# Kernel optimization log

Hardware: AMD Instinct MI355X
Metric: run time of the kernel (lower is better)

The kernel has to match this reference:

```python
import jax, jax.numpy as jnp
import numpy as np

NV = 16384
NF = 32768
B = 4


def _build_laplacian(nv, nf, seed=0):
    # Faithful replication of the torch module's __init__ laplacian construction.
    rng = np.random.RandomState(seed)
    faces = rng.randint(0, nv, size=(nf, 3)).astype(np.int64)
    lap = np.zeros((nv, nv), dtype=np.float32)
    lap[faces[:, 0], faces[:, 1]] = -1
    lap[faces[:, 1], faces[:, 0]] = -1
    lap[faces[:, 1], faces[:, 2]] = -1
    lap[faces[:, 2], faces[:, 1]] = -1
    lap[faces[:, 2], faces[:, 0]] = -1
    lap[faces[:, 0], faces[:, 2]] = -1
    r, c = np.diag_indices(nv)
    lap[r, c] = -lap.sum(1)
    deg = lap[r, c]  # degree per vertex (>= 0)
    # vectorized version of: for i: if lap[i,i] > 0: lap[i,:] /= lap[i,i]
    scale = np.where(deg > 0, 1.0 / np.maximum(deg, 1.0), 1.0).astype(np.float32)
    lap = lap * scale[:, None]
    return lap


def setup_inputs() -> dict:
    key = jax.random.key(0)
    x = jax.random.normal(key, (B, NV, 3), dtype=jnp.float32)
    laplacian = jnp.asarray(_build_laplacian(NV, NF))
    return {"x": x, "laplacian": laplacian}


def reference(x, laplacian):
    # y[b, i, d] = sum_j L[i, j] * x[b, j, d]
    y = jnp.einsum("ij,bjd->bid", laplacian, x)
    # squared L2 norm per batch element (sum over all non-batch dims)
    loss = jnp.sum(y * y, axis=(1, 2))  # [B]
    return loss
```

## Files before the change

### kernel.cpp

```cpp
#include <hip/hip_runtime.h>

#define NV 16384
#define BROWS 32
#define JT 256
#define NT (NV / JT)
#define THREADS 256

typedef const __attribute__((address_space(1))) void* as1_ptr;
typedef __attribute__((address_space(3))) void* as3_ptr;

__device__ __forceinline__ void gload_lds16(const float* g, float* l) {
  __builtin_amdgcn_global_load_lds((as1_ptr)g, (as3_ptr)l, 16, 0, 0);
}

#define FENCE asm volatile("" ::: "memory")
#define WAITV(n) asm volatile("s_waitcnt vmcnt(" #n ")" ::: "memory")

__global__ __launch_bounds__(THREADS, 2) void lap_loss_kernel(
    const float* __restrict__ x, const float* __restrict__ L,
    float* __restrict__ out) {
  __shared__ float lbuf[2][BROWS][JT];

  const int lane = threadIdx.x & 63;
  const int w    = threadIdx.x >> 6;
  const size_t i0 = (size_t)blockIdx.x * BROWS;

  const float* gL[8];
#pragma unroll
  for (int r = 0; r < 8; ++r)
    gL[r] = L + (i0 + 8 * w + r) * NV + lane * 4;

  const float* gx = x + (size_t)w * NV * 3 + lane * 12;

  float acc[BROWS][3];
#pragma unroll
  for (int r = 0; r < BROWS; ++r)
#pragma unroll
    for (int d = 0; d < 3; ++d) acc[r][d] = 0.f;

  float4 xc0 = *(const float4*)(gx + 0);
  float4 xc1 = *(const float4*)(gx + 4);
  float4 xc2 = *(const float4*)(gx + 8);
  FENCE;
#pragma unroll
  for (int r = 0; r < 8; ++r)
    gload_lds16(gL[r], &lbuf[0][8 * w + r][0]);
  FENCE;

#pragma unroll 1
  for (int t = 0; t < NT; ++t) {
    const int cur = t & 1;

    float4 xn0, xn1, xn2;
    if (t + 1 < NT) {
#pragma unroll
      for (int r = 0; r < 8; ++r)
        gload_lds16(gL[r] + (size_t)(t + 1) * JT, &lbuf[cur ^ 1][8 * w + r][0]);
      FENCE;
      const float* gxn = gx + (size_t)(t + 1) * JT * 3;
      xn0 = *(const float4*)(gxn + 0);
      xn1 = *(const float4*)(gxn + 4);
      xn2 = *(const float4*)(gxn + 8);
      FENCE;
      WAITV(11);
    } else {
      WAITV(0);
    }
    __builtin_amdgcn_s_barrier();
    FENCE;

    {
      const float xf[12] = {xc0.x, xc0.y, xc0.z, xc0.w,
                            xc1.x, xc1.y, xc1.z, xc1.w,
                            xc2.x, xc2.y, xc2.z, xc2.w};
#pragma unroll
      for (int r = 0; r < BROWS; ++r) {
        float4 lv = *(const float4*)&lbuf[cur][r][lane * 4];
        const float lf[4] = {lv.x, lv.y, lv.z, lv.w};
#pragma unroll
        for (int jj = 0; jj < 4; ++jj)
#pragma unroll
          for (int d = 0; d < 3; ++d)
            acc[r][d] = fmaf(lf[jj], xf[jj * 3 + d], acc[r][d]);
      }
    }

    FENCE;
    __builtin_amdgcn_s_barrier();
    FENCE;

    xc0 = xn0; xc1 = xn1; xc2 = xn2;
  }

  float s = 0.f;
#pragma unroll
  for (int r = 0; r < BROWS; ++r)
#pragma unroll
    for (int d = 0; d < 3; ++d) {
      float v = acc[r][d];
#pragma unroll
      for (int off = 32; off > 0; off >>= 1)
        v += __shfl_xor(v, off, 64);
      s += v * v;
    }

  if (lane == 0) atomicAdd(&out[w], s);
}

extern "C" void kernel_launch(void* const* d_in, const int* in_sizes, int n_in,
                              void* d_out, int out_size, void* d_ws, size_t ws_size,
                              hipStream_t stream) {
  const float* x = (const float*)d_in[0];
  const float* L = (const float*)d_in[1];
  float* out = (float*)d_out;

  hipMemsetAsync(out, 0, out_size * sizeof(float), stream);

  const int nblocks = NV / BROWS;
  lap_loss_kernel<<<nblocks, THREADS, 0, stream>>>(x, L, out);
}
```

Baseline: 229.3 us.

## Deepen L-tile prefetch to four stages and halve rows per block

Replaces the double-buffered LDS pipeline with a four-slot ring buffer that keeps three tiles in flight, issuing each tile three iterations ahead and waiting with matching vmcnt counts. Rows per block drop from 32 to 16, which doubles the grid and halves the accumulator registers. The aim is to hide more HBM latency on this bandwidth-bound streaming of the dense Laplacian. In exchange, x is now re-read by twice as many blocks and the hand-counted waitcnt values must exactly match the number of outstanding loads.

```diff
diff --git a/kernel.cpp b/kernel.cpp
--- a/kernel.cpp
+++ b/kernel.cpp
@@ -1,7 +1,7 @@
 #include <hip/hip_runtime.h>
 
 #define NV 16384
-#define BROWS 32
+#define BROWS 16
 #define JT 256
 #define NT (NV / JT)
 #define THREADS 256
@@ -15,20 +15,21 @@
 
 #define FENCE asm volatile("" ::: "memory")
 #define WAITV(n) asm volatile("s_waitcnt vmcnt(" #n ")" ::: "memory")
+#define BARRIER __builtin_amdgcn_s_barrier()
 
 __global__ __launch_bounds__(THREADS, 2) void lap_loss_kernel(
     const float* __restrict__ x, const float* __restrict__ L,
     float* __restrict__ out) {
-  __shared__ float lbuf[2][BROWS][JT];
+  __shared__ float lbuf[4][BROWS][JT];
 
   const int lane = threadIdx.x & 63;
   const int w    = threadIdx.x >> 6;
   const size_t i0 = (size_t)blockIdx.x * BROWS;
 
-  const float* gL[8];
-#pragma unroll
-  for (int r = 0; r < 8; ++r)
-    gL[r] = L + (i0 + 8 * w + r) * NV + lane * 4;
+  const float* gL0 = L + (i0 + 4 * w + 0) * NV + lane * 4;
+  const float* gL1 = L + (i0 + 4 * w + 1) * NV + lane * 4;
+  const float* gL2 = L + (i0 + 4 * w + 2) * NV + lane * 4;
+  const float* gL3 = L + (i0 + 4 * w + 3) * NV + lane * 4;
 
   const float* gx = x + (size_t)w * NV * 3 + lane * 12;
 
@@ -38,59 +39,72 @@
 #pragma unroll
     for (int d = 0; d < 3; ++d) acc[r][d] = 0.f;
 
-  float4 xc0 = *(const float4*)(gx + 0);
-  float4 xc1 = *(const float4*)(gx + 4);
-  float4 xc2 = *(const float4*)(gx + 8);
-  FENCE;
-#pragma unroll
-  for (int r = 0; r < 8; ++r)
-    gload_lds16(gL[r], &lbuf[0][8 * w + r][0]);
-  FENCE;
+  float4 xpf[4][3];
+
+#define ISSUE(T, S) do {                                               \
+    const float4* _p = (const float4*)(gx + (size_t)(T) * JT * 3);     \
+    xpf[S][0] = _p[0]; xpf[S][1] = _p[1]; xpf[S][2] = _p[2];           \
+    FENCE;                                                             \
+    gload_lds16(gL0 + (size_t)(T) * JT, &lbuf[S][4 * w + 0][0]);       \
+    gload_lds16(gL1 + (size_t)(T) * JT, &lbuf[S][4 * w + 1][0]);       \
+    gload_lds16(gL2 + (size_t)(T) * JT, &lbuf[S][4 * w + 2][0]);       \
+    gload_lds16(gL3 + (size_t)(T) * JT, &lbuf[S][4 * w + 3][0]);       \
+    FENCE;                                                             \
+  } while (0)
+
+#define COMPUTE(S) do {                                                \
+    const float xf[12] = {xpf[S][0].x, xpf[S][0].y, xpf[S][0].z,       \
+                          xpf[S][0].w, xpf[S][1].x, xpf[S][1].y,       \
+                          xpf[S][1].z, xpf[S][1].w, xpf[S][2].x,       \
+                          xpf[S][2].y, xpf[S][2].z, xpf[S][2].w};      \
+    _Pragma("unroll")                                                  \
+    for (int r = 0; r < BROWS; ++r) {                                  \
+      float4 lv = *(const float4*)&lbuf[S][r][lane * 4];               \
+      const float lf[4] = {lv.x, lv.y, lv.z, lv.w};                    \
+      _Pragma("unroll")                                                \
+      for (int q = 0; q < 4; ++q)                                      \
+        _Pragma("unroll")                                              \
+        for (int d = 0; d < 3; ++d)                                    \
+          acc[r][d] = fmaf(lf[q], xf[q * 3 + d], acc[r][d]);           \
+    }                                                                  \
+  } while (0)
+
+#define STEP_FULL(T, SI, SC) do {                                      \
+    ISSUE((T) + 3, SI);                                                \
+    WAITV(21);                                                         \
+    BARRIER; FENCE;                                                    \
+    COMPUTE(SC);                                                       \
+    FENCE; BARRIER; FENCE;                                             \
+  } while (0)
+
+  ISSUE(0, 0);
+  ISSUE(1, 1);
+  ISSUE(2, 2);
 
 #pragma unroll 1
-  for (int t = 0; t < NT; ++t) {
-    const int cur = t & 1;
+  for (int k = 0; k < 15; ++k) {
+    const int t = 4 * k;
+    STEP_FULL(t + 0, 3, 0);
+    STEP_FULL(t + 1, 0, 1);
+    STEP_FULL(t + 2, 1, 2);
+    STEP_FULL(t + 3, 2, 3);
+  }
 
-    float4 xn0, xn1, xn2;
-    if (t + 1 < NT) {
-#pragma unroll
-      for (int r = 0; r < 8; ++r)
-        gload_lds16(gL[r] + (size_t)(t + 1) * JT, &lbuf[cur ^ 1][8 * w + r][0]);
-      FENCE;
-      const float* gxn = gx + (size_t)(t + 1) * JT * 3;
-      xn0 = *(const float4*)(gxn + 0);
-      xn1 = *(const float4*)(gxn + 4);
-      xn2 = *(const float4*)(gxn + 8);
-      FENCE;
-      WAITV(11);
-    } else {
-      WAITV(0);
-    }
-    __builtin_amdgcn_s_barrier();
-    FENCE;
+  ISSUE(63, 3);
+  WAITV(21); BARRIER; FENCE;
+  COMPUTE(0);
+  FENCE; BARRIER; FENCE;
 
-    {
-      const float xf[12] = {xc0.x, xc0.y, xc0.z, xc0.w,
-                            xc1.x, xc1.y, xc1.z, xc1.w,
-                            xc2.x, xc2.y, xc2.z, xc2.w};
-#pragma unroll
-      for (int r = 0; r < BROWS; ++r) {
-        float4 lv = *(const float4*)&lbuf[cur][r][lane * 4];
-        const float lf[4] = {lv.x, lv.y, lv.z, lv.w};
-#pragma unroll
-        for (int jj = 0; jj < 4; ++jj)
-#pragma unroll
-          for (int d = 0; d < 3; ++d)
-            acc[r][d] = fmaf(lf[jj], xf[jj * 3 + d], acc[r][d]);
-      }
-    }
+  WAITV(14); BARRIER; FENCE;
+  COMPUTE(1);
+  FENCE; BARRIER; FENCE;
 
-    FENCE;
-    __builtin_amdgcn_s_barrier();
-    FENCE;
+  WAITV(7); BARRIER; FENCE;
+  COMPUTE(2);
+  FENCE; BARRIER; FENCE;
 
-    xc0 = xn0; xc1 = xn1; xc2 = xn2;
-  }
+  WAITV(0); BARRIER; FENCE;
+  COMPUTE(3);
 
   float s = 0.f;
 #pragma unroll
```

New measurement: 261.4 us. 14.0% more time.
